# Optimization experiments

Hardware: AMD Instinct MI355X
Metric: run time of the kernel (lower is better)

The kernel has to match this reference:

```python
import jax, jax.numpy as jnp
import numpy as np

CELLS = 56
EPS = 1e-9

def setup_inputs() -> dict:
    key = jax.random.key(0)
    k1, k2 = jax.random.split(key)
    B = 512
    F = CELLS * CELLS * 15  # 47040 floats per sample
    output = jax.random.uniform(k1, (B, F), dtype=jnp.float32)
    target = jax.random.uniform(k2, (B, F), dtype=jnp.float32)
    return {"output": output, "target": target}

def reference(output, target):
    B = output.shape[0]
    # reshape flat vector into [B, cells^2, 15] slots: x,y,w,h,conf,classes[5:14]
    o = output.reshape(B, CELLS * CELLS, 15)
    t = target.reshape(B, CELLS * CELLS, 15)
    # coordinate loss: only x (slice [i*15 : i*15+1]) plus sqrt(w)/sqrt(h) terms
    coord = (o[..., 0] - t[..., 0]) ** 2 \
          + (jnp.sqrt(o[..., 2]) - jnp.sqrt(t[..., 2])) ** 2 \
          + (jnp.sqrt(o[..., 3]) - jnp.sqrt(t[..., 3])) ** 2
    # binary cross-entropy on confidence (slot 4)
    conf = -(t[..., 4] * jnp.log(o[..., 4] + EPS)
             + (1.0 - t[..., 4]) * jnp.log(1.0 - o[..., 4] + EPS))
    # class loss: sum of squared diffs over slots 5:14 (9 elements)
    cls = jnp.sum((t[..., 5:14] - o[..., 5:14]) ** 2, axis=-1)
    # cell is counted only if output x-coordinate is nonzero (torch.is_nonzero gate)
    mask = o[..., 0] != 0
    per_cell = jnp.where(mask, coord + conf + cls, 0.0)
    return jnp.sum(per_cell)
```

## Files before the change

### kernel.cpp

```cpp
#include <hip/hip_runtime.h>


#define EPSF 1e-9f

__global__ __launch_bounds__(256) void yolo_loss_kernel(
    const float* __restrict__ o, const float* __restrict__ t,
    float* __restrict__ out_sum, int n4, int n)
{
    const int tid = threadIdx.x;
    const int stride = gridDim.x * 256;
    const float4* o4 = (const float4*)o;
    const float4* t4 = (const float4*)t;

    float acc = 0.f;

    #pragma unroll 2
    for (int i = blockIdx.x * 256 + tid; i < n4; i += stride) {
        const float4 ov = o4[i];
        const float4 tv = t4[i];

        const unsigned e0    = (unsigned)i * 4u;
        const unsigned cell0 = e0 / 15u;
        const unsigned slot0 = e0 - cell0 * 15u;
        const unsigned cell3 = (e0 + 3u) / 15u;
        const float g_lo = o[(size_t)cell0 * 15u];
        const float g_hi = o[(size_t)cell3 * 15u];

        const float oe[4] = {ov.x, ov.y, ov.z, ov.w};
        const float te[4] = {tv.x, tv.y, tv.z, tv.w};

        #pragma unroll
        for (int j = 0; j < 4; ++j) {
            unsigned s = slot0 + (unsigned)j;
            const bool wrap = s >= 15u;
            s = wrap ? s - 15u : s;
            const float gate = wrap ? g_hi : g_lo;
            const float ox = oe[j], tx = te[j];

            const bool issq = (s == 2u) | (s == 3u);
            const float a = issq ? sqrtf(ox) : ox;
            const float b = issq ? sqrtf(tx) : tx;
            const float d = a - b;
            const float sq = d * d;

            const float bce = -(tx * __logf(ox + EPSF)
                              + (1.f - tx) * __logf(1.f - ox + EPSF));

            float c = (s == 4u) ? bce : sq;
            c = (s == 1u || s == 14u) ? 0.f : c;
            c = (gate != 0.f) ? c : 0.f;
            acc += c;
        }
    }

    const int tail0 = n4 * 4;
    if (blockIdx.x == 0 && tid < n - tail0) {
        const unsigned e = (unsigned)(tail0 + tid);
        const unsigned cell = e / 15u;
        const unsigned s = e - cell * 15u;
        const float gate = o[(size_t)cell * 15u];
        const float ox = o[e], tx = t[e];
        const bool issq = (s == 2u) | (s == 3u);
        const float a = issq ? sqrtf(ox) : ox;
        const float b = issq ? sqrtf(tx) : tx;
        const float d = a - b;
        const float sq = d * d;
        const float bce = -(tx * __logf(ox + EPSF)
                          + (1.f - tx) * __logf(1.f - ox + EPSF));
        float c = (s == 4u) ? bce : sq;
        c = (s == 1u || s == 14u) ? 0.f : c;
        c = (gate != 0.f) ? c : 0.f;
        acc += c;
    }

    #pragma unroll
    for (int off = 32; off; off >>= 1) acc += __shfl_down(acc, off, 64);
    __shared__ float wsum[4];
    if ((tid & 63) == 0) wsum[tid >> 6] = acc;
    __syncthreads();
    if (tid == 0) atomicAdd(out_sum, wsum[0] + wsum[1] + wsum[2] + wsum[3]);
}

extern "C" void kernel_launch(void* const* d_in, const int* in_sizes, int n_in,
                              void* d_out, int out_size, void* d_ws, size_t ws_size,
                              hipStream_t stream) {
    const float* o = (const float*)d_in[0];
    const float* t = (const float*)d_in[1];
    float* out = (float*)d_out;
    const int n = in_sizes[0];
    const int n4 = n / 4;

    hipMemsetAsync(out, 0, sizeof(float), stream);

    const int grid = 2048;
    yolo_loss_kernel<<<grid, 256, 0, stream>>>(o, t, out, n4, n);
}
```

Measured before the change: 216.8 us.

## Add fully-unrolled fast path with batched loads and single BCE per float4

```diff
diff --git a/kernel.cpp b/kernel.cpp
--- a/kernel.cpp
+++ b/kernel.cpp
@@ -2,8 +2,89 @@
 
 
 #define EPSF 1e-9f
+#define LN2F 0.69314718055994530942f
 
-__global__ __launch_bounds__(256) void yolo_loss_kernel(
+__device__ __forceinline__ float bce_of(float ox, float tx) {
+    const float l1 = __log2f(ox + EPSF);
+    const float l2 = __log2f((1.f - ox) + EPSF);
+    return -LN2F * (tx * l1 + (1.f - tx) * l2);
+}
+
+__global__ __launch_bounds__(256, 4) void yolo_loss_fast(
+    const float* __restrict__ o, const float* __restrict__ t,
+    float* __restrict__ out_sum)
+{
+    const int tid = threadIdx.x;
+    const unsigned T   = gridDim.x * 256u;
+    const unsigned idx = blockIdx.x * 256u + (unsigned)tid;
+    const float4* o4 = (const float4*)o;
+    const float4* t4 = (const float4*)t;
+
+    float4 ob[8], tb[8];
+    float  gl[8], gh[8];
+    unsigned sl[8];
+    #pragma unroll
+    for (int k = 0; k < 8; ++k) {
+        const unsigned i  = idx + (unsigned)k * T;
+        const unsigned e0 = i * 4u;
+        const unsigned c0 = e0 / 15u;
+        const unsigned c3 = (e0 + 3u) / 15u;
+        sl[k] = e0 - c0 * 15u;
+        ob[k] = o4[i];
+        tb[k] = t4[i];
+        gl[k] = o[c0 * 15u];
+        gh[k] = o[c3 * 15u];
+    }
+    __builtin_amdgcn_sched_barrier(0);
+
+    float acc = 0.f;
+    #pragma unroll
+    for (int k = 0; k < 8; ++k) {
+        const unsigned s0 = sl[k];
+        const float glo = gl[k], ghi = gh[k];
+        const float oe[4] = {ob[k].x, ob[k].y, ob[k].z, ob[k].w};
+        const float te[4] = {tb[k].x, tb[k].y, tb[k].z, tb[k].w};
+
+        bool is4[4];
+        #pragma unroll
+        for (int j = 0; j < 4; ++j) {
+            const unsigned s = s0 + (unsigned)j;
+            is4[j] = (s == 4u) | (s == 19u);
+        }
+        float oc = oe[3], tc = te[3];
+        #pragma unroll
+        for (int j = 2; j >= 0; --j) { oc = is4[j] ? oe[j] : oc; tc = is4[j] ? te[j] : tc; }
+        const float bce = bce_of(oc, tc);
+
+        #pragma unroll
+        for (int j = 0; j < 4; ++j) {
+            unsigned s = s0 + (unsigned)j;
+            const bool wrap = s >= 15u;
+            s = wrap ? s - 15u : s;
+            const float gate = wrap ? ghi : glo;
+            const float ox = oe[j], tx = te[j];
+
+            const float d  = ox - tx;
+            const float sq = d * d;
+            const float s23 = (ox + tx) - 2.f * __builtin_amdgcn_sqrtf(ox * tx);
+
+            float c = ((s == 2u) | (s == 3u)) ? s23 : sq;
+            c = is4[j] ? bce : c;
+            c = ((s == 1u) | (s == 14u)) ? 0.f : c;
+            c = (gate != 0.f) ? c : 0.f;
+            acc += c;
+        }
+    }
+
+    #pragma unroll
+    for (int off = 32; off; off >>= 1) acc += __shfl_down(acc, off, 64);
+    __shared__ float wsum[4];
+    if ((tid & 63) == 0) wsum[tid >> 6] = acc;
+    __syncthreads();
+    if (tid == 0) atomicAdd(out_sum, wsum[0] + wsum[1] + wsum[2] + wsum[3]);
+}
+
+__global__ __launch_bounds__(256) void yolo_loss_generic(
     const float* __restrict__ o, const float* __restrict__ t,
     float* __restrict__ out_sum, int n4, int n)
 {
@@ -11,68 +92,50 @@
     const int stride = gridDim.x * 256;
     const float4* o4 = (const float4*)o;
     const float4* t4 = (const float4*)t;
-
     float acc = 0.f;
 
-    #pragma unroll 2
     for (int i = blockIdx.x * 256 + tid; i < n4; i += stride) {
         const float4 ov = o4[i];
         const float4 tv = t4[i];
-
-        const unsigned e0    = (unsigned)i * 4u;
-        const unsigned cell0 = e0 / 15u;
-        const unsigned slot0 = e0 - cell0 * 15u;
-        const unsigned cell3 = (e0 + 3u) / 15u;
-        const float g_lo = o[(size_t)cell0 * 15u];
-        const float g_hi = o[(size_t)cell3 * 15u];
-
+        const unsigned e0 = (unsigned)i * 4u;
+        const unsigned c0 = e0 / 15u;
+        const unsigned c3 = (e0 + 3u) / 15u;
+        const unsigned s0 = e0 - c0 * 15u;
+        const float glo = o[c0 * 15u], ghi = o[c3 * 15u];
         const float oe[4] = {ov.x, ov.y, ov.z, ov.w};
         const float te[4] = {tv.x, tv.y, tv.z, tv.w};
-
         #pragma unroll
         for (int j = 0; j < 4; ++j) {
-            unsigned s = slot0 + (unsigned)j;
+            unsigned s = s0 + (unsigned)j;
             const bool wrap = s >= 15u;
             s = wrap ? s - 15u : s;
-            const float gate = wrap ? g_hi : g_lo;
+            const float gate = wrap ? ghi : glo;
             const float ox = oe[j], tx = te[j];
-
-            const bool issq = (s == 2u) | (s == 3u);
-            const float a = issq ? sqrtf(ox) : ox;
-            const float b = issq ? sqrtf(tx) : tx;
-            const float d = a - b;
+            const float d = ox - tx;
             const float sq = d * d;
-
-            const float bce = -(tx * __logf(ox + EPSF)
-                              + (1.f - tx) * __logf(1.f - ox + EPSF));
-
-            float c = (s == 4u) ? bce : sq;
-            c = (s == 1u || s == 14u) ? 0.f : c;
+            const float s23 = (ox + tx) - 2.f * __builtin_amdgcn_sqrtf(ox * tx);
+            float c = ((s == 2u) | (s == 3u)) ? s23 : sq;
+            c = (s == 4u) ? bce_of(ox, tx) : c;
+            c = ((s == 1u) | (s == 14u)) ? 0.f : c;
             c = (gate != 0.f) ? c : 0.f;
             acc += c;
         }
     }
-
     const int tail0 = n4 * 4;
     if (blockIdx.x == 0 && tid < n - tail0) {
         const unsigned e = (unsigned)(tail0 + tid);
         const unsigned cell = e / 15u;
         const unsigned s = e - cell * 15u;
-        const float gate = o[(size_t)cell * 15u];
+        const float gate = o[cell * 15u];
         const float ox = o[e], tx = t[e];
-        const bool issq = (s == 2u) | (s == 3u);
-        const float a = issq ? sqrtf(ox) : ox;
-        const float b = issq ? sqrtf(tx) : tx;
-        const float d = a - b;
-        const float sq = d * d;
-        const float bce = -(tx * __logf(ox + EPSF)
-                          + (1.f - tx) * __logf(1.f - ox + EPSF));
-        float c = (s == 4u) ? bce : sq;
-        c = (s == 1u || s == 14u) ? 0.f : c;
+        const float d = ox - tx;
+        float c = d * d;
+        c = ((s == 2u) | (s == 3u)) ? (ox + tx) - 2.f * __builtin_amdgcn_sqrtf(ox * tx) : c;
+        c = (s == 4u) ? bce_of(ox, tx) : c;
+        c = ((s == 1u) | (s == 14u)) ? 0.f : c;
         c = (gate != 0.f) ? c : 0.f;
         acc += c;
     }
-
     #pragma unroll
     for (int off = 32; off; off >>= 1) acc += __shfl_down(acc, off, 64);
     __shared__ float wsum[4];
@@ -92,6 +155,10 @@
 
     hipMemsetAsync(out, 0, sizeof(float), stream);
 
-    const int grid = 2048;
-    yolo_loss_kernel<<<grid, 256, 0, stream>>>(o, t, out, n4, n);
+    if ((n % 4 == 0) && (n4 % (256 * 8) == 0)) {
+        const int grid = n4 / (256 * 8);
+        yolo_loss_fast<<<grid, 256, 0, stream>>>(o, t, out);
+    } else {
+        yolo_loss_generic<<<2940, 256, 0, stream>>>(o, t, out, n4, n);
+    }
 }
```

New measurement: 206.4 us. -4.8%, faster.
